# Optimization experiments

Hardware: AMD Instinct MI355X
Metric: run time of the kernel (lower is better)

The kernel has to match this reference:

```python
import jax, jax.numpy as jnp
import numpy as np

B, S, D_MODEL, H = 4, 2048, 1024, 16
DEPTH = D_MODEL // H  # 64


def setup_inputs() -> dict:
    key = jax.random.key(0)
    ks = jax.random.split(key, 12)
    inp = {
        "v": jax.random.normal(ks[0], (B, S, D_MODEL), jnp.float32),
        "k": jax.random.normal(ks[1], (B, S, D_MODEL), jnp.float32),
        "q": jax.random.normal(ks[2], (B, S, D_MODEL), jnp.float32),
        "mask": jnp.zeros((B, 1, 1, S), jnp.int32),  # unused by the layer
        # Dense(d_model) params (glorot-ish scale)
        "wq": jax.random.normal(ks[3], (D_MODEL, D_MODEL), jnp.float32) / np.sqrt(D_MODEL),
        "bq": jnp.zeros((D_MODEL,), jnp.float32),
        "wk": jax.random.normal(ks[4], (D_MODEL, D_MODEL), jnp.float32) / np.sqrt(D_MODEL),
        "bk": jnp.zeros((D_MODEL,), jnp.float32),
        "wv": jax.random.normal(ks[5], (D_MODEL, D_MODEL), jnp.float32) / np.sqrt(D_MODEL),
        "bv": jnp.zeros((D_MODEL,), jnp.float32),
        # global attention weights: [max_seq_len, 1], stddev=0.1
        "gqw": 0.1 * jax.random.normal(ks[6], (S, 1), jnp.float32),
        "gkw": 0.1 * jax.random.normal(ks[7], (S, 1), jnp.float32),
        "wo": jax.random.normal(ks[8], (D_MODEL, D_MODEL), jnp.float32) / np.sqrt(D_MODEL),
        "bo": jnp.zeros((D_MODEL,), jnp.float32),
    }
    return inp


def _split_heads(x):
    # [B, S, D] -> [B, H, S, depth]
    Bc = x.shape[0]
    return x.reshape(Bc, -1, H, DEPTH).transpose(0, 2, 1, 3)


def reference(v, k, q, mask, wq, bq, wk, bk, wv, bv, gqw, gkw, wo, bo):
    # QKV projections
    qh = _split_heads(q @ wq + bq)  # [B, H, S, depth]
    kh = _split_heads(k @ wk + bk)
    vh = _split_heads(v @ wv + bv)
    # Fastformer additive attention: mul -> seq-sum -> mul -> seq-sum -> mul -> add
    qh = qh * gqw                          # gqw [S,1] broadcasts over [B,H,S,depth]
    gq = jnp.sum(qh, axis=2, keepdims=True)  # global query [B,H,1,depth]
    kh = kh * gq * gkw
    gk = jnp.sum(kh, axis=2, keepdims=True)  # global key [B,H,1,depth]
    out = vh * gk + qh                       # [B,H,S,depth]
    # merge heads and output projection
    out = out.transpose(0, 2, 1, 3).reshape(out.shape[0], -1, D_MODEL)
    return out @ wo + bo
```

## Files before the change

kernel.cpp:

```cpp
#include <hip/hip_runtime.h>

#define DM 1024
#define BATCH 4
#define SEQ 2048
#define M_TOT (BATCH*SEQ)

typedef unsigned short ushort_t;
typedef __bf16 bf16x8 __attribute__((ext_vector_type(8)));
typedef float f32x4 __attribute__((ext_vector_type(4)));
typedef unsigned short u16x8 __attribute__((ext_vector_type(8)));

__device__ __forceinline__ ushort_t f2bf(float f) {
  unsigned u = __builtin_bit_cast(unsigned, f);
  u = (u + 0x7fffu + ((u >> 16) & 1u)) >> 16;
  return (ushort_t)u;
}
__device__ __forceinline__ float bf2f(ushort_t h) {
  unsigned u = ((unsigned)h) << 16;
  return __builtin_bit_cast(float, u);
}

#define GLL(gp, lp)                                                            \
  __builtin_amdgcn_global_load_lds(                                            \
      (const __attribute__((address_space(1))) unsigned int*)(const void*)(gp),\
      (__attribute__((address_space(3))) unsigned int*)(void*)(lp), 16, 0, 0)

__device__ __forceinline__ size_t src_off(int row0, int e) {
  return (size_t)(row0 + (e >> 2)) * DM + (((e & 3) ^ ((e >> 3) & 3)) * 8);
}

__global__ void k_reduce(const float* __restrict__ q, const float* __restrict__ k,
                         const float* __restrict__ v,
                         const float* __restrict__ gqw, const float* __restrict__ gkw,
                         float* __restrict__ qr, float* __restrict__ kr,
                         float* __restrict__ G,
                         ushort_t* __restrict__ qb, ushort_t* __restrict__ vb) {
  const int b = blockIdx.x, dch = blockIdx.y, sch = blockIdx.z;
  const int d = dch * 256 + threadIdx.x;
  const int s0 = sch * (SEQ / 16);
  const size_t base = ((size_t)b * SEQ + s0) * DM + d;
  const float* qp = q + base;
  const float* kp = k + base;
  const float* vp = v + base;
  float aq = 0.f, ak = 0.f;
  for (int i = 0; i < SEQ / 16; ++i) {
    const float w = gqw[s0 + i];
    const float qv = qp[(size_t)i * DM];
    aq += w * qv;
    ak += gkw[s0 + i] * kp[(size_t)i * DM];
    qb[base + (size_t)i * DM] = f2bf(w * qv);
    vb[base + (size_t)i * DM] = f2bf(vp[(size_t)i * DM]);
  }
  atomicAdd(&qr[b * DM + d], aq);
  atomicAdd(&kr[b * DM + d], ak);
  if (b == 0 && dch == 0 && threadIdx.x < SEQ / 16) {
    atomicAdd(&G[0], gqw[s0 + threadIdx.x]);
    atomicAdd(&G[1], gkw[s0 + threadIdx.x]);
  }
}

__global__ void k_gpart(const float* __restrict__ wq, const float* __restrict__ wk,
                        const float* __restrict__ qr, const float* __restrict__ kr,
                        float* __restrict__ qacc, float* __restrict__ kacc) {
  const int d = blockIdx.x * 256 + threadIdx.x;
  const int k0 = blockIdx.y * 32;
  __shared__ float sq[4][32], sk[4][32];
  if (threadIdx.x < 128) {
    const int b = threadIdx.x >> 5, kk = threadIdx.x & 31;
    sq[b][kk] = qr[b * DM + k0 + kk];
    sk[b][kk] = kr[b * DM + k0 + kk];
  }
  __syncthreads();
  float aq[4] = {0.f, 0.f, 0.f, 0.f}, ak[4] = {0.f, 0.f, 0.f, 0.f};
#pragma unroll 8
  for (int kk = 0; kk < 32; ++kk) {
    const float wqv = wq[(size_t)(k0 + kk) * DM + d];
    const float wkv = wk[(size_t)(k0 + kk) * DM + d];
#pragma unroll
    for (int b = 0; b < 4; ++b) {
      aq[b] += sq[b][kk] * wqv;
      ak[b] += sk[b][kk] * wkv;
    }
  }
#pragma unroll
  for (int b = 0; b < 4; ++b) {
    atomicAdd(&qacc[b * DM + d], aq[b]);
    atomicAdd(&kacc[b * DM + d], ak[b]);
  }
}

__global__ void k_gfin(const float* __restrict__ qacc, const float* __restrict__ kacc,
                       const float* __restrict__ bq, const float* __restrict__ bk,
                       const float* __restrict__ G, float* __restrict__ gk) {
  const int i = blockIdx.x * 256 + threadIdx.x;
  const int d = i & (DM - 1);
  const float gqv = qacc[i] + bq[d] * G[0];
  const float gkr = kacc[i] + bk[d] * G[1];
  gk[i] = gqv * gkr;
}

__global__ void k_conv(const float* __restrict__ x0, ushort_t* __restrict__ y0,
                       const float* __restrict__ x1, ushort_t* __restrict__ y1) {
  const float* x = blockIdx.y ? x1 : x0;
  ushort_t* y = blockIdx.y ? y1 : y0;
  size_t i = (size_t)blockIdx.x * 256 + threadIdx.x;
  const float4* p = (const float4*)x + i * 2;
  float4 a = p[0], b = p[1];
  u16x8 o;
  o[0] = f2bf(a.x); o[1] = f2bf(a.y); o[2] = f2bf(a.z); o[3] = f2bf(a.w);
  o[4] = f2bf(b.x); o[5] = f2bf(b.y); o[6] = f2bf(b.z); o[7] = f2bf(b.w);
  *(u16x8*)(y + i * 8) = o;
}

__global__ void k_trans(const float* __restrict__ W, ushort_t* __restrict__ T) {
  __shared__ float ls[32][33];
  const int bi = blockIdx.x, bj = blockIdx.y;
#pragma unroll
  for (int p = 0; p < 4; ++p) {
    int e = threadIdx.x + p * 256;
    int r = e >> 5, c = e & 31;
    ls[r][c] = W[(size_t)(bi * 32 + r) * DM + bj * 32 + c];
  }
  __syncthreads();
#pragma unroll
  for (int p = 0; p < 4; ++p) {
    int e = threadIdx.x + p * 256;
    int r = e >> 5, c = e & 31;
    T[(size_t)(bj * 32 + r) * DM + bi * 32 + c] = f2bf(ls[c][r]);
  }
}

__global__ void k_wog(const ushort_t* __restrict__ woT, const float* __restrict__ gk,
                      ushort_t* __restrict__ wogT) {
  const size_t i = (size_t)blockIdx.x * 256 + threadIdx.x;
  const size_t c = i * 8;
  const int j0 = (int)(c & (DM - 1));
  const int b = (int)(c >> 20);
  u16x8 wv = *(const u16x8*)(woT + (c & ((1u << 20) - 1)));
  const float4 g0 = *(const float4*)(gk + b * DM + j0);
  const float4 g1 = *(const float4*)(gk + b * DM + j0 + 4);
  float g[8] = {g0.x, g0.y, g0.z, g0.w, g1.x, g1.y, g1.z, g1.w};
  u16x8 o;
#pragma unroll
  for (int j = 0; j < 8; ++j) o[j] = f2bf(bf2f(wv[j]) * g[j]);
  *(u16x8*)(wogT + i * 8) = o;
}

__global__ void k_bias(const float* __restrict__ wo, const float* __restrict__ bq,
                       const float* __restrict__ bv, const float* __restrict__ gk,
                       float* __restrict__ qbias, float* __restrict__ vbias) {
  const int n = blockIdx.x * 256 + threadIdx.x;
  const int k0 = blockIdx.y * 32;
  float aq = 0.f, av[4] = {0.f, 0.f, 0.f, 0.f};
  for (int kk = 0; kk < 32; ++kk) {
    const float w = wo[(size_t)(k0 + kk) * DM + n];
    aq += bq[k0 + kk] * w;
    const float bw = bv[k0 + kk] * w;
#pragma unroll
    for (int b = 0; b < 4; ++b) av[b] += bw * gk[b * DM + k0 + kk];
  }
  atomicAdd(&qbias[n], aq);
#pragma unroll
  for (int b = 0; b < 4; ++b) atomicAdd(&vbias[b * DM + n], av[b]);
}

__global__ void k_small(const ushort_t* __restrict__ woT, const ushort_t* __restrict__ wogT,
                        const ushort_t* __restrict__ wqB, const ushort_t* __restrict__ wvB,
                        ushort_t* __restrict__ WqoT, ushort_t* __restrict__ WvbT) {
  __shared__ __align__(16) ushort_t lsA[3][128 * 32];
  __shared__ __align__(16) ushort_t lsB[3][128 * 32];
  const int z = blockIdx.z;
  const ushort_t* A  = z == 0 ? woT : wogT + (size_t)(z - 1) * (DM * DM);
  const ushort_t* Bt = z == 0 ? wqB : wvB;
  ushort_t* Out      = z == 0 ? WqoT : WvbT + (size_t)(z - 1) * (DM * DM);

  const int tid = threadIdx.x;
  const int w = tid >> 6, lane = tid & 63;
  const int m0 = blockIdx.x * 128, n0 = blockIdx.y * 128;
  const int wr = w >> 1, wc = w & 1;
  const int c0 = w * 2, c1 = c0 + 1;
  const int e0 = c0 * 64 + lane, e1 = c1 * 64 + lane;
  const ushort_t* gA0 = A + src_off(m0, e0);
  const ushort_t* gA1 = A + src_off(m0, e1);
  const ushort_t* gB0 = Bt + src_off(n0, e0);
  const ushort_t* gB1 = Bt + src_off(n0, e1);

  int aoff[4], boff[4];
#pragma unroll
  for (int i = 0; i < 4; ++i) {
    const int ra = wr * 64 + i * 16 + (lane & 15);
    aoff[i] = ra * 32 + (((lane >> 4) ^ ((ra >> 1) & 3)) * 8);
    const int rb = wc * 64 + i * 16 + (lane & 15);
    boff[i] = rb * 32 + (((lane >> 4) ^ ((rb >> 1) & 3)) * 8);
  }

  f32x4 acc[4][4];
#pragma unroll
  for (int i = 0; i < 4; ++i)
#pragma unroll
    for (int j = 0; j < 4; ++j) acc[i][j] = (f32x4){0.f, 0.f, 0.f, 0.f};

  auto STAGE = [&](int tt, int buf) {
    const int o = tt * 32;
    GLL(gA0 + o, &lsA[buf][c0 * 512]);
    GLL(gA1 + o, &lsA[buf][c1 * 512]);
    GLL(gB0 + o, &lsB[buf][c0 * 512]);
    GLL(gB1 + o, &lsB[buf][c1 * 512]);
  };

  STAGE(0, 0);
  STAGE(1, 1);
#pragma unroll 1
  for (int t = 0; t < 32; ++t) {
    if (t < 31) { asm volatile("s_waitcnt vmcnt(4)" ::: "memory"); }
    else        { asm volatile("s_waitcnt vmcnt(0)" ::: "memory"); }
    __builtin_amdgcn_s_barrier();
    if (t + 2 < 32) STAGE(t + 2, (t + 2) % 3);
    const int cur = t % 3;
    bf16x8 av[4], bv[4];
#pragma unroll
    for (int i = 0; i < 4; ++i) av[i] = *(const bf16x8*)(&lsA[cur][aoff[i]]);
#pragma unroll
    for (int j = 0; j < 4; ++j) bv[j] = *(const bf16x8*)(&lsB[cur][boff[j]]);
#pragma unroll
    for (int i = 0; i < 4; ++i)
#pragma unroll
      for (int j = 0; j < 4; ++j)
        acc[i][j] = __builtin_amdgcn_mfma_f32_16x16x32_bf16(av[i], bv[j], acc[i][j], 0, 0, 0);
  }

  const int lr = (lane >> 4) * 4, lc = lane & 15;
  const int rbase = m0 + wr * 64, cbase = n0 + wc * 64;
#pragma unroll
  for (int j = 0; j < 4; ++j) {
    const int col = cbase + j * 16 + lc;
#pragma unroll
    for (int i = 0; i < 4; ++i)
#pragma unroll
      for (int t = 0; t < 4; ++t)
        Out[(size_t)(rbase + i * 16 + lr + t) * DM + col] = f2bf(acc[i][j][t]);
  }
}

__global__ void k_big(const ushort_t* __restrict__ qb, const ushort_t* __restrict__ vb,
                      const ushort_t* __restrict__ WqoT, const ushort_t* __restrict__ WvbT,
                      const float* __restrict__ gqw, const float* __restrict__ qbias,
                      const float* __restrict__ vbias, const float* __restrict__ bo,
                      float* __restrict__ Out) {
  __shared__ __align__(16) ushort_t lsA[3][128 * 32];
  __shared__ __align__(16) ushort_t lsB[3][128 * 32];
  const int tid = threadIdx.x;
  const int w = tid >> 6, lane = tid & 63;
  const int bid = blockIdx.x;
  const int lg = (bid & 7) * 64 + (bid >> 3);
  const int m0 = (lg & 63) * 128, n0 = (lg >> 6) * 128;
  const int b = m0 >> 11;
  const int wr = w >> 1, wc = w & 1;
  const int c0 = w * 2, c1 = c0 + 1;
  const int e0 = c0 * 64 + lane, e1 = c1 * 64 + lane;
  const size_t oA0 = src_off(m0, e0), oA1 = src_off(m0, e1);
  const size_t oB0 = src_off(n0, e0), oB1 = src_off(n0, e1);
  const ushort_t* gAq0 = qb + oA0;
  const ushort_t* gAq1 = qb + oA1;
  const ushort_t* gAv0 = vb + oA0;
  const ushort_t* gAv1 = vb + oA1;
  const ushort_t* gBq0 = WqoT + oB0;
  const ushort_t* gBq1 = WqoT + oB1;
  const ushort_t* gBv0 = WvbT + (size_t)b * (DM * DM) + oB0;
  const ushort_t* gBv1 = WvbT + (size_t)b * (DM * DM) + oB1;

  int aoff[4], boff[4];
#pragma unroll
  for (int i = 0; i < 4; ++i) {
    const int ra = wr * 64 + i * 16 + (lane & 15);
    aoff[i] = ra * 32 + (((lane >> 4) ^ ((ra >> 1) & 3)) * 8);
    const int rb = wc * 64 + i * 16 + (lane & 15);
    boff[i] = rb * 32 + (((lane >> 4) ^ ((rb >> 1) & 3)) * 8);
  }

  f32x4 acc[4][4];
#pragma unroll
  for (int i = 0; i < 4; ++i)
#pragma unroll
    for (int j = 0; j < 4; ++j) acc[i][j] = (f32x4){0.f, 0.f, 0.f, 0.f};

  auto STAGE = [&](int tt, int buf) {
    const ushort_t *a0, *a1, *b0, *b1;
    if (tt < 32) {
      const int o = tt * 32;
      a0 = gAq0 + o; a1 = gAq1 + o; b0 = gBq0 + o; b1 = gBq1 + o;
    } else {
      const int o = (tt - 32) * 32;
      a0 = gAv0 + o; a1 = gAv1 + o; b0 = gBv0 + o; b1 = gBv1 + o;
    }
    GLL(a0, &lsA[buf][c0 * 512]);
    GLL(a1, &lsA[buf][c1 * 512]);
    GLL(b0, &lsB[buf][c0 * 512]);
    GLL(b1, &lsB[buf][c1 * 512]);
  };

  STAGE(0, 0);
  STAGE(1, 1);
#pragma unroll 1
  for (int t = 0; t < 64; ++t) {
    if (t < 63) { asm volatile("s_waitcnt vmcnt(4)" ::: "memory"); }
    else        { asm volatile("s_waitcnt vmcnt(0)" ::: "memory"); }
    __builtin_amdgcn_s_barrier();
    if (t + 2 < 64) STAGE(t + 2, (t + 2) % 3);
    const int cur = t % 3;
    bf16x8 av[4], bv[4];
#pragma unroll
    for (int i = 0; i < 4; ++i) av[i] = *(const bf16x8*)(&lsA[cur][aoff[i]]);
#pragma unroll
    for (int j = 0; j < 4; ++j) bv[j] = *(const bf16x8*)(&lsB[cur][boff[j]]);
#pragma unroll
    for (int i = 0; i < 4; ++i)
#pragma unroll
      for (int j = 0; j < 4; ++j)
        acc[i][j] = __builtin_amdgcn_mfma_f32_16x16x32_bf16(av[i], bv[j], acc[i][j], 0, 0, 0);
  }

  const int lr = (lane >> 4) * 4, lc = lane & 15;
  const int rbase = m0 + wr * 64, cbase = n0 + wc * 64;
#pragma unroll
  for (int j = 0; j < 4; ++j) {
    const int col = cbase + j * 16 + lc;
    const float qbn = qbias[col];
    const float cb = vbias[b * DM + col] + bo[col];
#pragma unroll
    for (int i = 0; i < 4; ++i)
#pragma unroll
      for (int t = 0; t < 4; ++t) {
        const int row = rbase + i * 16 + lr + t;
        Out[(size_t)row * DM + col] = acc[i][j][t] + gqw[row & (SEQ - 1)] * qbn + cb;
      }
  }
}

extern "C" void kernel_launch(void* const* d_in, const int* in_sizes, int n_in,
                              void* d_out, int out_size, void* d_ws, size_t ws_size,
                              hipStream_t stream) {
  const float* v   = (const float*)d_in[0];
  const float* k   = (const float*)d_in[1];
  const float* q   = (const float*)d_in[2];
  const float* wq  = (const float*)d_in[4];
  const float* bq  = (const float*)d_in[5];
  const float* wk  = (const float*)d_in[6];
  const float* bk  = (const float*)d_in[7];
  const float* wv  = (const float*)d_in[8];
  const float* bv  = (const float*)d_in[9];
  const float* gqw = (const float*)d_in[10];
  const float* gkw = (const float*)d_in[11];
  const float* wo  = (const float*)d_in[12];
  const float* bo  = (const float*)d_in[13];
  float* out = (float*)d_out;
  float* wsf = (float*)d_ws;

  float* qr    = wsf + 0;
  float* kr    = wsf + 4096;
  float* qacc  = wsf + 8192;
  float* kacc  = wsf + 12288;
  float* G     = wsf + 16384;
  float* qbias = wsf + 16640;
  float* vbias = wsf + 17664;
  float* gk    = wsf + 21760;
  ushort_t* b16  = (ushort_t*)((char*)d_ws + (1 << 17));
  ushort_t* qb   = b16;
  ushort_t* vb   = qb + (size_t)M_TOT * DM;
  ushort_t* wqB  = vb + (size_t)M_TOT * DM;
  ushort_t* wvB  = wqB + (size_t)DM * DM;
  ushort_t* woT  = wvB + (size_t)DM * DM;
  ushort_t* WqoT = woT + (size_t)DM * DM;
  ushort_t* WvbT = WqoT + (size_t)DM * DM;
  ushort_t* wogT = (ushort_t*)out;

  hipMemsetAsync(d_ws, 0, 21760 * sizeof(float), stream);

  k_conv<<<dim3((DM * DM / 8) / 256, 2), 256, 0, stream>>>(wq, wqB, wv, wvB);
  k_trans<<<dim3(32, 32), 256, 0, stream>>>(wo, woT);

  k_reduce<<<dim3(BATCH, DM / 256, 16), 256, 0, stream>>>(q, k, v, gqw, gkw, qr, kr, G, qb, vb);

  k_gpart<<<dim3(DM / 256, DM / 32), 256, 0, stream>>>(wq, wk, qr, kr, qacc, kacc);
  k_gfin<<<(BATCH * DM) / 256, 256, 0, stream>>>(qacc, kacc, bq, bk, G, gk);

  k_wog<<<(BATCH * DM * DM / 8) / 256, 256, 0, stream>>>(woT, gk, wogT);
  k_bias<<<dim3(DM / 256, DM / 32), 256, 0, stream>>>(wo, bq, bv, gk, qbias, vbias);

  k_small<<<dim3(8, 8, 5), 256, 0, stream>>>(woT, wogT, wqB, wvB, WqoT, WvbT);

  k_big<<<dim3(512), 256, 0, stream>>>(
      qb, vb, WqoT, WvbT, gqw, qbias, vbias, bo, out);
}
```

Baseline: 142.2 us.

## Enlarge k_big GEMM tile to 256x128 with 512 threads and K-step 64

The main fused GEMM kernel now uses a 256x128 output tile per block with 8 waves instead of 128x128 with 4 waves. The K step per pipeline stage grows from 32 to 64, which halves the number of barrier iterations. The raw row-major global loads use a new XOR-swizzled LDS layout. The grid drops from 512 to 256 blocks, which improves reuse of B-tiles and amortises sync cost, but uses more LDS and only one block per CU. That may leave some CUs idle with 256 blocks on 256 CUs.

```diff
diff --git a/kernel.cpp b/kernel.cpp
--- a/kernel.cpp
+++ b/kernel.cpp
@@ -242,40 +242,45 @@
   }
 }
 
-__global__ void k_big(const ushort_t* __restrict__ qb, const ushort_t* __restrict__ vb,
-                      const ushort_t* __restrict__ WqoT, const ushort_t* __restrict__ WvbT,
-                      const float* __restrict__ gqw, const float* __restrict__ qbias,
-                      const float* __restrict__ vbias, const float* __restrict__ bo,
-                      float* __restrict__ Out) {
-  __shared__ __align__(16) ushort_t lsA[3][128 * 32];
-  __shared__ __align__(16) ushort_t lsB[3][128 * 32];
+__global__ __launch_bounds__(512, 1)
+void k_big(const ushort_t* __restrict__ qb, const ushort_t* __restrict__ vb,
+           const ushort_t* __restrict__ WqoT, const ushort_t* __restrict__ WvbT,
+           const float* __restrict__ gqw, const float* __restrict__ qbias,
+           const float* __restrict__ vbias, const float* __restrict__ bo,
+           float* __restrict__ Out) {
+  __shared__ __align__(16) ushort_t lsA[3][256 * 64];
+  __shared__ __align__(16) ushort_t lsB[3][128 * 64];
   const int tid = threadIdx.x;
   const int w = tid >> 6, lane = tid & 63;
-  const int bid = blockIdx.x;
-  const int lg = (bid & 7) * 64 + (bid >> 3);
-  const int m0 = (lg & 63) * 128, n0 = (lg >> 6) * 128;
+  const int m0 = blockIdx.x * 256, n0 = blockIdx.y * 128;
   const int b = m0 >> 11;
   const int wr = w >> 1, wc = w & 1;
-  const int c0 = w * 2, c1 = c0 + 1;
-  const int e0 = c0 * 64 + lane, e1 = c1 * 64 + lane;
-  const size_t oA0 = src_off(m0, e0), oA1 = src_off(m0, e1);
-  const size_t oB0 = src_off(n0, e0), oB1 = src_off(n0, e1);
-  const ushort_t* gAq0 = qb + oA0;
-  const ushort_t* gAq1 = qb + oA1;
-  const ushort_t* gAv0 = vb + oA0;
-  const ushort_t* gAv1 = vb + oA1;
-  const ushort_t* gBq0 = WqoT + oB0;
-  const ushort_t* gBq1 = WqoT + oB1;
-  const ushort_t* gBv0 = WvbT + (size_t)b * (DM * DM) + oB0;
-  const ushort_t* gBv1 = WvbT + (size_t)b * (DM * DM) + oB1;
-
-  int aoff[4], boff[4];
+
+  const int subrow = lane >> 3;
+  const int srcslot = (lane & 7) ^ subrow;
+  size_t offA[4], offB[2];
+#pragma unroll
+  for (int p = 0; p < 4; ++p) {
+    const int row = (4 * w + p) * 8 + subrow;
+    offA[p] = (size_t)(m0 + row) * DM + srcslot * 8;
+  }
+#pragma unroll
+  for (int p = 0; p < 2; ++p) {
+    const int row = (2 * w + p) * 8 + subrow;
+    offB[p] = (size_t)(n0 + row) * DM + srcslot * 8;
+  }
+  const ushort_t* Bv = WvbT + (size_t)b * (DM * DM);
+
+  const int g = lane >> 4, l7 = lane & 7, l15 = lane & 15;
+  int aoff0[4], aoff1[4], boff0[4], boff1[4];
 #pragma unroll
   for (int i = 0; i < 4; ++i) {
-    const int ra = wr * 64 + i * 16 + (lane & 15);
-    aoff[i] = ra * 32 + (((lane >> 4) ^ ((ra >> 1) & 3)) * 8);
-    const int rb = wc * 64 + i * 16 + (lane & 15);
-    boff[i] = rb * 32 + (((lane >> 4) ^ ((rb >> 1) & 3)) * 8);
+    const int ra = wr * 64 + i * 16 + l15;
+    aoff0[i] = ra * 64 + ((g ^ l7) * 8);
+    aoff1[i] = ra * 64 + (((4 + g) ^ l7) * 8);
+    const int rb = wc * 64 + i * 16 + l15;
+    boff0[i] = rb * 64 + ((g ^ l7) * 8);
+    boff1[i] = rb * 64 + (((4 + g) ^ l7) * 8);
   }
 
   f32x4 acc[4][4];
@@ -285,39 +290,52 @@
     for (int j = 0; j < 4; ++j) acc[i][j] = (f32x4){0.f, 0.f, 0.f, 0.f};
 
   auto STAGE = [&](int tt, int buf) {
-    const ushort_t *a0, *a1, *b0, *b1;
-    if (tt < 32) {
-      const int o = tt * 32;
-      a0 = gAq0 + o; a1 = gAq1 + o; b0 = gBq0 + o; b1 = gBq1 + o;
-    } else {
-      const int o = (tt - 32) * 32;
-      a0 = gAv0 + o; a1 = gAv1 + o; b0 = gBv0 + o; b1 = gBv1 + o;
-    }
-    GLL(a0, &lsA[buf][c0 * 512]);
-    GLL(a1, &lsA[buf][c1 * 512]);
-    GLL(b0, &lsB[buf][c0 * 512]);
-    GLL(b1, &lsB[buf][c1 * 512]);
+    const ushort_t* Ab;
+    const ushort_t* Bb;
+    int k0;
+    if (tt < 16) { Ab = qb; Bb = WqoT; k0 = tt * 64; }
+    else         { Ab = vb; Bb = Bv;   k0 = (tt - 16) * 64; }
+#pragma unroll
+    for (int p = 0; p < 4; ++p)
+      GLL(Ab + offA[p] + k0, &lsA[buf][(4 * w + p) * 512]);
+#pragma unroll
+    for (int p = 0; p < 2; ++p)
+      GLL(Bb + offB[p] + k0, &lsB[buf][(2 * w + p) * 512]);
   };
 
   STAGE(0, 0);
   STAGE(1, 1);
 #pragma unroll 1
-  for (int t = 0; t < 64; ++t) {
-    if (t < 63) { asm volatile("s_waitcnt vmcnt(4)" ::: "memory"); }
+  for (int t = 0; t < 32; ++t) {
+    if (t < 31) { asm volatile("s_waitcnt vmcnt(6)" ::: "memory"); }
     else        { asm volatile("s_waitcnt vmcnt(0)" ::: "memory"); }
     __builtin_amdgcn_s_barrier();
-    if (t + 2 < 64) STAGE(t + 2, (t + 2) % 3);
+    if (t + 2 < 32) STAGE(t + 2, (t + 2) % 3);
     const int cur = t % 3;
-    bf16x8 av[4], bv[4];
-#pragma unroll
-    for (int i = 0; i < 4; ++i) av[i] = *(const bf16x8*)(&lsA[cur][aoff[i]]);
-#pragma unroll
-    for (int j = 0; j < 4; ++j) bv[j] = *(const bf16x8*)(&lsB[cur][boff[j]]);
-#pragma unroll
-    for (int i = 0; i < 4; ++i)
-#pragma unroll
-      for (int j = 0; j < 4; ++j)
-        acc[i][j] = __builtin_amdgcn_mfma_f32_16x16x32_bf16(av[i], bv[j], acc[i][j], 0, 0, 0);
+    {
+      bf16x8 av[4], bv[4];
+#pragma unroll
+      for (int i = 0; i < 4; ++i) av[i] = *(const bf16x8*)(&lsA[cur][aoff0[i]]);
+#pragma unroll
+      for (int j = 0; j < 4; ++j) bv[j] = *(const bf16x8*)(&lsB[cur][boff0[j]]);
+#pragma unroll
+      for (int i = 0; i < 4; ++i)
+#pragma unroll
+        for (int j = 0; j < 4; ++j)
+          acc[i][j] = __builtin_amdgcn_mfma_f32_16x16x32_bf16(av[i], bv[j], acc[i][j], 0, 0, 0);
+    }
+    {
+      bf16x8 av[4], bv[4];
+#pragma unroll
+      for (int i = 0; i < 4; ++i) av[i] = *(const bf16x8*)(&lsA[cur][aoff1[i]]);
+#pragma unroll
+      for (int j = 0; j < 4; ++j) bv[j] = *(const bf16x8*)(&lsB[cur][boff1[j]]);
+#pragma unroll
+      for (int i = 0; i < 4; ++i)
+#pragma unroll
+        for (int j = 0; j < 4; ++j)
+          acc[i][j] = __builtin_amdgcn_mfma_f32_16x16x32_bf16(av[i], bv[j], acc[i][j], 0, 0, 0);
+    }
   }
 
   const int lr = (lane >> 4) * 4, lc = lane & 15;
@@ -389,6 +407,6 @@
 
   k_small<<<dim3(8, 8, 5), 256, 0, stream>>>(woT, wogT, wqB, wvB, WqoT, WvbT);
 
-  k_big<<<dim3(512), 256, 0, stream>>>(
+  k_big<<<dim3(M_TOT / 256, DM / 128), 512, 0, stream>>>(
       qb, vb, WqoT, WvbT, gqw, qbias, vbias, bo, out);
 }
```

Result: faster. 136.8 us (-3.8%).
